# Optimization experiments

Hardware: AMD Instinct MI355X
Metric: run time of the kernel (lower is better)

Reference implementation:

```python
import jax, jax.numpy as jnp
import numpy as np

B, S, H, V = 64, 256, 1024, 10000


def setup_inputs() -> dict:
    key = jax.random.key(0)
    ks = jax.random.split(key, 16)
    s = 1.0 / np.sqrt(H)
    return {
        "input_seq": jax.random.randint(ks[0], (B,), 0, V),
        "last_hidden": jax.random.normal(ks[1], (1, 1, H), jnp.float32),
        "encoder_outputs": jax.random.normal(ks[2], (S, B, H), jnp.float32),
        "emb_table": jax.random.normal(ks[3], (V, H), jnp.float32) * s,
        "W_ih": jax.random.normal(ks[4], (3 * H, H), jnp.float32) * s,
        "W_hh": jax.random.normal(ks[5], (3 * H, H), jnp.float32) * s,
        "b_ih": jax.random.normal(ks[6], (3 * H,), jnp.float32) * s,
        "b_hh": jax.random.normal(ks[7], (3 * H,), jnp.float32) * s,
        "W_attn": jax.random.normal(ks[8], (H, 2 * H), jnp.float32) * s,
        "b_attn": jax.random.normal(ks[9], (H,), jnp.float32) * s,
        "v_attn": jax.random.normal(ks[10], (H,), jnp.float32) * s,
        "W_concat": jax.random.normal(ks[11], (H, 2 * H), jnp.float32) * s,
        "b_concat": jax.random.normal(ks[12], (H,), jnp.float32) * s,
        "W_out": jax.random.normal(ks[13], (V, H), jnp.float32) * s,
        "b_out": jax.random.normal(ks[14], (V,), jnp.float32) * s,
    }


def _gru_scan(x_seq, h0, W_ih, W_hh, b_ih, b_hh):
    # x_seq: [T, H] (here T == batch dim, per the module's batch_first quirk)
    def step(h, x):
        gi = x @ W_ih.T + b_ih   # [3H]
        gh = h @ W_hh.T + b_hh   # [3H]
        ir, iz, inn = jnp.split(gi, 3)
        hr, hz, hn = jnp.split(gh, 3)
        r = jax.nn.sigmoid(ir + hr)
        z = jax.nn.sigmoid(iz + hz)
        n = jnp.tanh(inn + r * hn)
        h_new = (1.0 - z) * n + z * h
        return h_new, h_new

    h_last, outs = jax.lax.scan(step, h0, x_seq)
    return outs, h_last


def reference(input_seq, last_hidden, encoder_outputs, emb_table, W_ih, W_hh,
              b_ih, b_hh, W_attn, b_attn, v_attn, W_concat, b_concat, W_out, b_out):
    embedded = emb_table[input_seq]                       # [B, H]
    # GRU fed [1, B, H] with batch_first=True -> recurs over B with one hidden
    rnn_output, h_last = _gru_scan(embedded, last_hidden[0, 0], W_ih, W_hh, b_ih, b_hh)
    hidden = h_last[None, None, :]                        # [1, 1, H]

    # concat attention: score(b,i) = v . (W_attn @ [h_b ; enc_ib] + b_attn)
    enc = jnp.transpose(encoder_outputs, (1, 0, 2))       # [B, S, H]
    h_bc = jnp.broadcast_to(rnn_output[:, None, :], (B, S, H))
    cat = jnp.concatenate([h_bc, enc], axis=-1)           # [B, S, 2H]
    energy = jnp.einsum('bsk,hk->bsh', cat, W_attn) + b_attn
    scores = jnp.einsum('bsh,h->bs', energy, v_attn)      # [B, S]
    attn_weights = jax.nn.softmax(scores, axis=-1)[:, None, :]  # [B, 1, S]

    context = jnp.einsum('bs,bsh->bh', attn_weights[:, 0, :], enc)  # [B, H]
    concat_input = jnp.concatenate([rnn_output, context], axis=-1)  # [B, 2H]
    concat_output = jnp.tanh(concat_input @ W_concat.T + b_concat)  # [B, H]
    output = concat_output @ W_out.T + b_out                        # [B, V]
    return output, hidden, attn_weights
```

## Files before the change

kernel.cpp:

```cpp
#include <hip/hip_runtime.h>
#include <math.h>

#define kH  1024
#define kB  64
#define kS  256
#define kV  10000
#define kH3 3072

typedef unsigned long long u64;

__device__ __forceinline__ float warp_sum(float v) {
#pragma unroll
  for (int off = 32; off > 0; off >>= 1) v += __shfl_down(v, off, 64);
  return v;
}
__device__ __forceinline__ float warp_max_all(float v) {
#pragma unroll
  for (int off = 32; off > 0; off >>= 1) v = fmaxf(v, __shfl_xor(v, off, 64));
  return v;
}
__device__ __forceinline__ float warp_sum_all(float v) {
#pragma unroll
  for (int off = 32; off > 0; off >>= 1) v += __shfl_xor(v, off, 64);
  return v;
}
__device__ __forceinline__ float sigmoidf_(float x) {
  return __fdividef(1.0f, 1.0f + __expf(-x));
}
__device__ __forceinline__ float tanhf_(float x) {
  const float t = __expf(-2.0f * fabsf(x));
  const float r = __fdividef(1.0f - t, 1.0f + t);
  return copysignf(r, x);
}

__global__ __launch_bounds__(256) void k_pre(const int* __restrict__ seq,
    const float* __restrict__ emb, const float* __restrict__ W_ih,
    const float* __restrict__ b_ih, const float* __restrict__ W_attn,
    const float* __restrict__ v_attn, float* __restrict__ GI,
    float* __restrict__ w2h) {
  __shared__ float4 red[256];
  if (blockIdx.x < 768) {
    const int lane = threadIdx.x & 63;
    const int r = blockIdx.x * 4 + (threadIdx.x >> 6);
    const float4* wp = (const float4*)(W_ih + (size_t)r * kH) + lane * 4;
    const float4 w0 = wp[0], w1 = wp[1], w2 = wp[2], w3 = wp[3];
    const float br = b_ih[r];
    for (int t = 0; t < kB; ++t) {
      const int tok = seq[t];
      const float4* xp = (const float4*)(emb + (size_t)tok * kH) + lane * 4;
      const float4 x0 = xp[0], x1 = xp[1], x2 = xp[2], x3 = xp[3];
      float acc = w0.x*x0.x + w0.y*x0.y + w0.z*x0.z + w0.w*x0.w;
      acc += w1.x*x1.x + w1.y*x1.y + w1.z*x1.z + w1.w*x1.w;
      acc += w2.x*x2.x + w2.y*x2.y + w2.z*x2.z + w2.w*x2.w;
      acc += w3.x*x3.x + w3.y*x3.y + w3.z*x3.z + w3.w*x3.w;
      acc = warp_sum(acc);
      if (lane == 0) GI[(size_t)t * kH3 + r] = acc + br;
    }
  } else {
    const int t  = threadIdx.x;
    const int wb = blockIdx.x - 768;
    const int k0 = kH + wb * 4;
    float ax = 0, ay = 0, az = 0, aw = 0;
    for (int h = t; h < kH; h += 256) {
      const float vh = v_attn[h];
      const float4 wq = *(const float4*)(W_attn + (size_t)h * 2048 + k0);
      ax += vh * wq.x; ay += vh * wq.y; az += vh * wq.z; aw += vh * wq.w;
    }
    red[t] = make_float4(ax, ay, az, aw);
    __syncthreads();
    for (int s = 128; s > 0; s >>= 1) {
      if (t < s) {
        const float4 a = red[t], b = red[t + s];
        red[t] = make_float4(a.x + b.x, a.y + b.y, a.z + b.z, a.w + b.w);
      }
      __syncthreads();
    }
    if (t == 0) *(float4*)(w2h + wb * 4) = red[0];
  }
}

__global__ __launch_bounds__(256) void k_gru(const float* __restrict__ h0,
    const float* __restrict__ W_hh, const float* __restrict__ b_hh,
    const float* __restrict__ GI, float* __restrict__ rnn,
    u64* __restrict__ step) {
  __shared__ float4 wlds4[12 * 256];
  __shared__ __align__(16) float hs[2][kH];
  const int tid  = threadIdx.x;
  const int lane = tid & 63;
  const int w    = tid >> 6;
  const int bid  = blockIdx.x;
  const int j    = bid * 4 + w;

#pragma unroll
  for (int c = 0; c < 12; ++c) {
    const int f    = c * 256 + tid;
    const int row  = f >> 8;
    const int col4 = f & 255;
    const int q    = row >> 2, r = row & 3;
    wlds4[f] = ((const float4*)(W_hh + ((size_t)q * kH + bid * 4 + r) * kH))[col4];
  }

  const float bhr = b_hh[j];
  const float bhz = b_hh[kH + j];
  const float bhn = b_hh[2 * kH + j];

  for (int t = 0; t < kB; ++t) {
    float gir = GI[(size_t)t * kH3 + j];
    float giz = GI[(size_t)t * kH3 + kH + j];
    float gin = GI[(size_t)t * kH3 + 2 * kH + j];
    asm volatile("" :: "v"(gir), "v"(giz), "v"(gin));

    float* hb = hs[t & 1];
    if (t == 0) {
      ((float4*)hb)[tid] = ((const float4*)h0)[tid];
    } else {
      const u64* sb = step + (size_t)(t - 1) * kH;
      const unsigned want = (unsigned)t;
      const int i0 = tid * 4;
      bool done[4] = {false, false, false, false};
      float v[4];
      while (true) {
        bool all = true;
#pragma unroll
        for (int k = 0; k < 4; ++k) {
          if (!done[k]) {
            const u64 x = __hip_atomic_load(&sb[i0 + k],
                __ATOMIC_RELAXED, __HIP_MEMORY_SCOPE_AGENT);
            if ((unsigned)(x >> 32) == want) {
              v[k] = __uint_as_float((unsigned)x);
              done[k] = true;
            } else {
              all = false;
            }
          }
        }
        if (all) break;
        __builtin_amdgcn_s_sleep(1);
      }
#pragma unroll
      for (int k = 0; k < 4; ++k) hb[i0 + k] = v[k];
    }
    __syncthreads();

    float4 hx4[4];
#pragma unroll
    for (int c = 0; c < 4; ++c) hx4[c] = ((const float4*)hb)[lane + 64 * c];

    float d[3];
#pragma unroll
    for (int q = 0; q < 3; ++q) {
      float acc = 0.f;
#pragma unroll
      for (int c = 0; c < 4; ++c) {
        const float4 wq = wlds4[(q * 4 + w) * 256 + lane + 64 * c];
        const float4 h4 = hx4[c];
        acc += wq.x * h4.x + wq.y * h4.y + wq.z * h4.z + wq.w * h4.w;
      }
      d[q] = acc;
    }
#pragma unroll
    for (int q = 0; q < 3; ++q) d[q] = warp_sum(d[q]);

    if (lane == 0) {
      const float ho = hb[j];
      const float r = sigmoidf_(gir + d[0] + bhr);
      const float z = sigmoidf_(giz + d[1] + bhz);
      const float n = tanhf_(gin + r * (d[2] + bhn));
      const float hn = (1.f - z) * n + z * ho;
      rnn[(size_t)t * kH + j] = hn;
      __hip_atomic_store(&step[(size_t)t * kH + j],
                         (((u64)(t + 1)) << 32) | __float_as_uint(hn),
                         __ATOMIC_RELAXED, __HIP_MEMORY_SCOPE_AGENT);
    }
  }
}

__global__ __launch_bounds__(1024) void k_att(const float* __restrict__ enc,
    const float* __restrict__ w2h, const float* __restrict__ rnn,
    float* __restrict__ attn, float* __restrict__ ctx,
    float* __restrict__ hid) {
  __shared__ float scl[kS];
  __shared__ float sm[4], ss[4];
  __shared__ float4 part4[1024];
  const int b = blockIdx.x, tid = threadIdx.x;
  const int lane = tid & 63, w = tid >> 6;

  {
    const float4* wp = (const float4*)w2h + lane * 4;
    const float4 wq0 = wp[0], wq1 = wp[1], wq2 = wp[2], wq3 = wp[3];
    for (int k = 0; k < 16; ++k) {
      const int s = w * 16 + k;
      const float4* ep =
          (const float4*)(enc + ((size_t)s * kB + b) * kH) + lane * 4;
      const float4 e0 = ep[0], e1 = ep[1], e2 = ep[2], e3 = ep[3];
      float acc = e0.x*wq0.x + e0.y*wq0.y + e0.z*wq0.z + e0.w*wq0.w;
      acc += e1.x*wq1.x + e1.y*wq1.y + e1.z*wq1.z + e1.w*wq1.w;
      acc += e2.x*wq2.x + e2.y*wq2.y + e2.z*wq2.z + e2.w*wq2.w;
      acc += e3.x*wq3.x + e3.y*wq3.y + e3.z*wq3.z + e3.w*wq3.w;
      acc = warp_sum(acc);
      if (lane == 0) scl[s] = acc;
    }
  }
  __syncthreads();

  float x = 0.f, e = 0.f;
  if (tid < kS) {
    x = scl[tid];
    const float m = warp_max_all(x);
    if (lane == 0) sm[w] = m;
  }
  __syncthreads();
  if (tid < kS) {
    const float m = fmaxf(fmaxf(sm[0], sm[1]), fmaxf(sm[2], sm[3]));
    e = __expf(x - m);
    const float s = warp_sum_all(e);
    if (lane == 0) ss[w] = s;
  }
  __syncthreads();
  if (tid < kS) {
    const float s = ss[0] + ss[1] + ss[2] + ss[3];
    const float a = e / s;
    attn[b * kS + tid] = a;
    scl[tid] = a;
  }
  if (b < 4 && tid < kS) {
    hid[b * kS + tid] = rnn[63 * kH + b * kS + tid];
  }
  __syncthreads();

  const int hc = tid & 255;
  const int sq = tid >> 8;
  const float4* encb = (const float4*)enc;
  float4 acc = make_float4(0.f, 0.f, 0.f, 0.f);
  const int s0 = sq * 64;
#pragma unroll 4
  for (int s = s0; s < s0 + 64; ++s) {
    const float a = scl[s];
    const float4 v = encb[((size_t)s * kB + b) * 256 + hc];
    acc.x += a * v.x; acc.y += a * v.y; acc.z += a * v.z; acc.w += a * v.w;
  }
  part4[tid] = acc;
  __syncthreads();
  if (tid < 256) {
    const float4 p0 = part4[tid], p1 = part4[tid + 256];
    const float4 p2 = part4[tid + 512], p3 = part4[tid + 768];
    float4 r;
    r.x = p0.x + p1.x + p2.x + p3.x;
    r.y = p0.y + p1.y + p2.y + p3.y;
    r.z = p0.z + p1.z + p2.z + p3.z;
    r.w = p0.w + p1.w + p2.w + p3.w;
    ((float4*)(ctx + (size_t)b * kH))[tid] = r;
  }
}

__global__ __launch_bounds__(256) void k_concat(const float* __restrict__ rnn,
    const float* __restrict__ ctx, const float* __restrict__ W_c,
    const float* __restrict__ b_c, float* __restrict__ coT) {
  const int lane = threadIdx.x & 63;
  const int iq = blockIdx.x >> 2;
  const int bq = blockIdx.x & 3;
  const int i  = iq * 4 + (threadIdx.x >> 6);
  float wreg[32];
  {
    const float4* wp = (const float4*)(W_c + (size_t)i * 2048) + lane * 8;
#pragma unroll
    for (int c = 0; c < 8; ++c) {
      const float4 f = wp[c];
      wreg[c * 4 + 0] = f.x; wreg[c * 4 + 1] = f.y;
      wreg[c * 4 + 2] = f.z; wreg[c * 4 + 3] = f.w;
    }
  }
  const float bc = b_c[i];
  const int jcol = lane * 32;
  const float* xbase = (jcol < kH) ? (rnn + jcol) : (ctx + (jcol - kH));
  for (int b = bq * 16; b < bq * 16 + 16; ++b) {
    const float* xr = xbase + (size_t)b * kH;
    float acc = 0.f;
#pragma unroll
    for (int c = 0; c < 8; ++c) {
      const float4 x = *(const float4*)(xr + c * 4);
      acc += wreg[c * 4 + 0] * x.x + wreg[c * 4 + 1] * x.y +
             wreg[c * 4 + 2] * x.z + wreg[c * 4 + 3] * x.w;
    }
    acc = warp_sum(acc);
    if (lane == 0) coT[(size_t)i * kB + b] = tanhf(acc + bc);
  }
}

__global__ __launch_bounds__(256) void k_out(const float* __restrict__ coT,
    const float* __restrict__ W_out, const float* __restrict__ b_out,
    float* __restrict__ out) {
  __shared__ float wlds[16 * kH];
  const int v0 = blockIdx.x * 16;
  {
    const float4* src = (const float4*)(W_out + (size_t)v0 * kH);
    float4 tmp[16];
#pragma unroll
    for (int c = 0; c < 16; ++c) tmp[c] = src[threadIdx.x + 256 * c];
    float4* dst = (float4*)wlds;
#pragma unroll
    for (int c = 0; c < 16; ++c) dst[threadIdx.x + 256 * c] = tmp[c];
  }
  __syncthreads();

  const int lane = threadIdx.x & 63;
  const int w    = threadIdx.x >> 6;
  float acc[4] = {0.f, 0.f, 0.f, 0.f};
#pragma unroll 2
  for (int h = 0; h < kH; h += 4) {
    const float x0 = coT[(size_t)(h + 0) * kB + lane];
    const float x1 = coT[(size_t)(h + 1) * kB + lane];
    const float x2 = coT[(size_t)(h + 2) * kB + lane];
    const float x3 = coT[(size_t)(h + 3) * kB + lane];
#pragma unroll
    for (int vi = 0; vi < 4; ++vi) {
      const float4 wq = *(const float4*)&wlds[(w * 4 + vi) * kH + h];
      acc[vi] += wq.x * x0 + wq.y * x1 + wq.z * x2 + wq.w * x3;
    }
  }
  const float4 bq = *(const float4*)(b_out + v0 + w * 4);
  float4 r;
  r.x = acc[0] + bq.x; r.y = acc[1] + bq.y;
  r.z = acc[2] + bq.z; r.w = acc[3] + bq.w;
  *(float4*)&out[(size_t)lane * kV + v0 + w * 4] = r;
}

extern "C" void kernel_launch(void* const* d_in, const int* in_sizes, int n_in,
                              void* d_out, int out_size, void* d_ws,
                              size_t ws_size, hipStream_t stream) {
  const int*   seq    = (const int*)  d_in[0];
  const float* h0     = (const float*)d_in[1];
  const float* enc    = (const float*)d_in[2];
  const float* emb    = (const float*)d_in[3];
  const float* W_ih   = (const float*)d_in[4];
  const float* W_hh   = (const float*)d_in[5];
  const float* b_ih   = (const float*)d_in[6];
  const float* b_hh   = (const float*)d_in[7];
  const float* W_attn = (const float*)d_in[8];
  const float* v_attn = (const float*)d_in[10];
  const float* W_conc = (const float*)d_in[11];
  const float* b_conc = (const float*)d_in[12];
  const float* W_outp = (const float*)d_in[13];
  const float* b_outp = (const float*)d_in[14];

  float* out      = (float*)d_out;
  float* out_hid  = out + 640000;
  float* out_attn = out + 641024;

  float* ws = (float*)d_ws;
  float* GI   = ws;
  float* RNN  = ws + 196608;
  u64*   STEP = (u64*)(ws + 262144);
  float* W2H  = ws + 393216;
  float* CTX  = ws + 394240;
  float* COT  = ws + 459776;

  k_pre<<<1024, 256, 0, stream>>>(seq, emb, W_ih, b_ih, W_attn, v_attn,
                                  GI, W2H);
  k_gru<<<256, 256, 0, stream>>>(h0, W_hh, b_hh, GI, RNN, STEP);
  k_att<<<64, 1024, 0, stream>>>(enc, W2H, RNN, out_attn, CTX, out_hid);
  k_concat<<<1024, 256, 0, stream>>>(RNN, CTX, W_conc, b_conc, COT);
  k_out<<<625, 256, 0, stream>>>(COT, W_outp, b_outp, out);
}
```

Before: 540.5 us.

## Tile input-gate GEMM in k_pre through shared memory for embedding reuse

Rewrites the W_ih × embedded projection in k_pre as a shared-memory tiled GEMM. Each block now computes 16 gate rows for all 64 tokens, staging 64-wide K chunks of the gathered embeddings (transposed, padded) and weights in LDS. Before, every row re-read all 64 embedding rows from global memory. The block count drops from 1024 to 448, with fewer blocks doing more work each and two barriers per K chunk.

New measurement: 542.2 us. No clear change (+0.3%).

```diff
diff --git a/kernel.cpp b/kernel.cpp
--- a/kernel.cpp
+++ b/kernel.cpp
@@ -38,44 +38,80 @@
     const float* __restrict__ b_ih, const float* __restrict__ W_attn,
     const float* __restrict__ v_attn, float* __restrict__ GI,
     float* __restrict__ w2h) {
+  __shared__ float xl[64 * 65];
+  __shared__ float wl[16 * 64];
   __shared__ float4 red[256];
-  if (blockIdx.x < 768) {
-    const int lane = threadIdx.x & 63;
-    const int r = blockIdx.x * 4 + (threadIdx.x >> 6);
-    const float4* wp = (const float4*)(W_ih + (size_t)r * kH) + lane * 4;
-    const float4 w0 = wp[0], w1 = wp[1], w2 = wp[2], w3 = wp[3];
-    const float br = b_ih[r];
-    for (int t = 0; t < kB; ++t) {
-      const int tok = seq[t];
-      const float4* xp = (const float4*)(emb + (size_t)tok * kH) + lane * 4;
-      const float4 x0 = xp[0], x1 = xp[1], x2 = xp[2], x3 = xp[3];
-      float acc = w0.x*x0.x + w0.y*x0.y + w0.z*x0.z + w0.w*x0.w;
-      acc += w1.x*x1.x + w1.y*x1.y + w1.z*x1.z + w1.w*x1.w;
-      acc += w2.x*x2.x + w2.y*x2.y + w2.z*x2.z + w2.w*x2.w;
-      acc += w3.x*x3.x + w3.y*x3.y + w3.z*x3.z + w3.w*x3.w;
-      acc = warp_sum(acc);
-      if (lane == 0) GI[(size_t)t * kH3 + r] = acc + br;
-    }
+  const int tid = threadIdx.x;
+
+  if (blockIdx.x < 192) {
+    const int rblk = blockIdx.x * 16;
+    const int t = tid & 63;
+    const int g = tid >> 6;
+    float acc[4] = {0.f, 0.f, 0.f, 0.f};
+
+    for (int c = 0; c < 16; ++c) {
+      const int h0 = c * 64;
+      {
+        const int tx = tid >> 2;
+        const int tok = seq[tx];
+        const float* xr = emb + (size_t)tok * kH + h0;
+#pragma unroll
+        for (int k = 0; k < 4; ++k) {
+          const int slot = (tid & 3) + 4 * k;
+          const float4 v = *(const float4*)(xr + slot * 4);
+          const int hh = slot * 4;
+          xl[(hh + 0) * 65 + tx] = v.x;
+          xl[(hh + 1) * 65 + tx] = v.y;
+          xl[(hh + 2) * 65 + tx] = v.z;
+          xl[(hh + 3) * 65 + tx] = v.w;
+        }
+      }
+      {
+        const int r = tid >> 4, c4 = tid & 15;
+        *(float4*)&wl[r * 64 + c4 * 4] =
+            ((const float4*)(W_ih + (size_t)(rblk + r) * kH + h0))[c4];
+      }
+      __syncthreads();
+#pragma unroll
+      for (int q = 0; q < 16; ++q) {
+        const int hh = q * 4;
+        const float x0 = xl[(hh + 0) * 65 + t];
+        const float x1 = xl[(hh + 1) * 65 + t];
+        const float x2 = xl[(hh + 2) * 65 + t];
+        const float x3 = xl[(hh + 3) * 65 + t];
+#pragma unroll
+        for (int i = 0; i < 4; ++i) {
+          const float4 wq = *(const float4*)&wl[(g * 4 + i) * 64 + hh];
+          acc[i] += wq.x * x0 + wq.y * x1 + wq.z * x2 + wq.w * x3;
+        }
+      }
+      __syncthreads();
+    }
+    const float4 bi = *(const float4*)(b_ih + rblk + g * 4);
+    float4 o;
+    o.x = acc[0] + bi.x; o.y = acc[1] + bi.y;
+    o.z = acc[2] + bi.z; o.w = acc[3] + bi.w;
+    *(float4*)(GI + (size_t)t * kH3 + rblk + g * 4) = o;
+
   } else {
-    const int t  = threadIdx.x;
-    const int wb = blockIdx.x - 768;
+    const int wb = blockIdx.x - 192;
     const int k0 = kH + wb * 4;
     float ax = 0, ay = 0, az = 0, aw = 0;
-    for (int h = t; h < kH; h += 256) {
+    for (int h = tid; h < kH; h += 256) {
       const float vh = v_attn[h];
       const float4 wq = *(const float4*)(W_attn + (size_t)h * 2048 + k0);
       ax += vh * wq.x; ay += vh * wq.y; az += vh * wq.z; aw += vh * wq.w;
     }
-    red[t] = make_float4(ax, ay, az, aw);
+    red[tid] = make_float4(ax, ay, az, aw);
     __syncthreads();
     for (int s = 128; s > 0; s >>= 1) {
-      if (t < s) {
-        const float4 a = red[t], b = red[t + s];
-        red[t] = make_float4(a.x + b.x, a.y + b.y, a.z + b.z, a.w + b.w);
+      if (tid < s) {
+        const float4 a = red[tid], b = red[tid + s];
+        red[tid] = make_float4(a.x + b.x, a.y + b.y, a.z + b.z, a.w + b.w);
       }
       __syncthreads();
     }
-    if (t == 0) *(float4*)(w2h + wb * 4) = red[0];
+    if (tid == 0) *(float4*)(w2h + wb * 4) = red[0];
   }
 }
 
@@ -355,8 +391,8 @@
   float* CTX  = ws + 394240;
   float* COT  = ws + 459776;
 
-  k_pre<<<1024, 256, 0, stream>>>(seq, emb, W_ih, b_ih, W_attn, v_attn,
-                                  GI, W2H);
+  k_pre<<<448, 256, 0, stream>>>(seq, emb, W_ih, b_ih, W_attn, v_attn,
+                                 GI, W2H);
   k_gru<<<256, 256, 0, stream>>>(h0, W_hh, b_hh, GI, RNN, STEP);
   k_att<<<64, 1024, 0, stream>>>(enc, W2H, RNN, out_attn, CTX, out_hid);
   k_concat<<<1024, 256, 0, stream>>>(RNN, CTX, W_conc, b_conc, COT);
```
